# Optimization experiments

Hardware: AMD Instinct MI355X
Metric: run time of the kernel (lower is better)

The kernel has to match this reference:

```python
import jax, jax.numpy as jnp
import numpy as np

B, S, D = 2, 2048, 1024
H, DQK, DV = 16, 64, 64

def setup_inputs() -> dict:
    key = jax.random.key(0)
    k1, k2, k3, k4, k5 = jax.random.split(key, 5)
    scale_in = 1.0 / np.sqrt(D)
    scale_v = 1.0 / np.sqrt(H * DV)
    return {
        "x":   jax.random.normal(k1, (B, S, D), dtype=jnp.float32),
        "W_q": jax.random.uniform(k2, (D, H * DQK), minval=-scale_in, maxval=scale_in, dtype=jnp.float32),
        "W_k": jax.random.uniform(k3, (D, H * DQK), minval=-scale_in, maxval=scale_in, dtype=jnp.float32),
        "W_v": jax.random.uniform(k4, (D, H * DV), minval=-scale_in, maxval=scale_in, dtype=jnp.float32),
        "W_o": jax.random.uniform(k5, (H * DV, D), minval=-scale_v, maxval=scale_v, dtype=jnp.float32),
    }

def reference(x, W_q, W_k, W_v, W_o):
    b, s, _ = x.shape
    # projections -> [B, H, S, d]
    Q = (x @ W_q).reshape(b, s, H, DQK).transpose(0, 2, 1, 3)
    K = (x @ W_k).reshape(b, s, H, DQK).transpose(0, 2, 1, 3)
    V = (x @ W_v).reshape(b, s, H, DV).transpose(0, 2, 1, 3)
    scores = jnp.einsum('bhqd,bhkd->bhqk', Q, K) / np.sqrt(DQK).astype(np.float32)
    causal_mask = jnp.triu(jnp.ones((s, s), dtype=bool), k=1)  # True above diagonal
    scores = jnp.where(causal_mask[None, None], -jnp.inf, scores)
    attn = jax.nn.softmax(scores, axis=-1)
    out = jnp.einsum('bhqk,bhkd->bhqd', attn, V)  # [B,H,S,DV]
    out = out.transpose(0, 2, 1, 3).reshape(b, s, H * DV)
    return out @ W_o
```

## Files before the change

kernel.cpp:

```cpp
#include <hip/hip_runtime.h>


typedef float  f32x4  __attribute__((ext_vector_type(4)));
typedef __bf16 bf16x8 __attribute__((ext_vector_type(8)));

__device__ __forceinline__ unsigned short f2bf(float f) {
    __bf16 h = (__bf16)f;
    return __builtin_bit_cast(unsigned short, h);
}

__device__ __forceinline__ void gld16(unsigned short* lds, const unsigned short* g) {
    __builtin_amdgcn_global_load_lds(
        (const __attribute__((address_space(1))) void*)g,
        (__attribute__((address_space(3))) void*)lds, 16, 0, 0);
}

__global__ __launch_bounds__(256) void castx(const float* __restrict__ x,
                                             unsigned short* __restrict__ xb) {
    size_t i = ((size_t)blockIdx.x * 256 + threadIdx.x) * 4;
    float4 v = *(const float4*)(x + i);
    ushort4 o;
    o.x = f2bf(v.x); o.y = f2bf(v.y); o.z = f2bf(v.z); o.w = f2bf(v.w);
    *(ushort4*)(xb + i) = o;
}

__global__ __launch_bounds__(256) void wtrans(const float* __restrict__ W0,
                                              const float* __restrict__ W1,
                                              const float* __restrict__ W2,
                                              const float* __restrict__ W3,
                                              unsigned short* __restrict__ WT) {
    __shared__ float T[64][65];
    const int z = blockIdx.z;
    const float* W = (z == 0) ? W0 : (z == 1) ? W1 : (z == 2) ? W2 : W3;
    const int k0 = blockIdx.y * 64, n0 = blockIdx.x * 64;
    const int tid = threadIdx.x;
#pragma unroll
    for (int i = 0; i < 4; i++) {
        int c = tid + i * 256;
        int r = c >> 4, col = (c & 15) * 4;
        float4 v = *(const float4*)(W + (size_t)(k0 + r) * 1024 + n0 + col);
        T[r][col] = v.x; T[r][col + 1] = v.y; T[r][col + 2] = v.z; T[r][col + 3] = v.w;
    }
    __syncthreads();
    unsigned short* out = WT + (size_t)z * 1024 * 1024;
#pragma unroll
    for (int i = 0; i < 2; i++) {
        int c = tid + i * 256;
        int nr = c >> 3, koff = (c & 7) * 8;
        union { unsigned short us[8]; uint4 v; } pk;
#pragma unroll
        for (int j = 0; j < 8; j++) pk.us[j] = f2bf(T[koff + j][nr]);
        *(uint4*)(out + (size_t)(n0 + nr) * 1024 + k0 + koff) = pk.v;
    }
}

__global__ __launch_bounds__(256) void gemm_qkv(const unsigned short* __restrict__ A,
                                                const unsigned short* __restrict__ WTall,
                                                unsigned short* __restrict__ outq,
                                                unsigned short* __restrict__ Vp) {
    __shared__ unsigned short As[128 * 32];
    __shared__ unsigned short Bs[128 * 32];
    const int tid = threadIdx.x;
    const int w = tid >> 6, lane = tid & 63, quad = lane >> 4, ln = lane & 15;

    const int blk = blockIdx.x;
    const int n0 = ((blk >> 3) & 7) * 128;
    const int g  = ((blk >> 6) << 3) | (blk & 7);
    const int z  = g >> 5;
    const int m0 = (g & 31) * 128;

    const unsigned short* BT = WTall + (size_t)z * (1024 * 1024);
    const float scl = (z == 0) ? 0.180336878f : 1.0f;
    const bool swp = (z < 2);

    const int lr = lane >> 2;
    const int lc = ((lane & 3) ^ (lr & 3)) * 8;
    const int fsw = (quad ^ (ln & 3)) * 8;

    const f32x4 z4 = {0.f, 0.f, 0.f, 0.f};
    f32x4 acc[4][4];
#pragma unroll
    for (int i = 0; i < 4; i++)
#pragma unroll
        for (int j = 0; j < 4; j++) acc[i][j] = z4;

    const int wm = (w & 1) * 64, wn = (w >> 1) * 64;
    const int R0 = w * 32, R1 = w * 32 + 16;

    for (int k0 = 0; k0 < 1024; k0 += 32) {
        __syncthreads();
        gld16(As + R0 * 32, A  + (size_t)(m0 + R0 + lr) * 1024 + k0 + lc);
        gld16(As + R1 * 32, A  + (size_t)(m0 + R1 + lr) * 1024 + k0 + lc);
        gld16(Bs + R0 * 32, BT + (size_t)(n0 + R0 + lr) * 1024 + k0 + lc);
        gld16(Bs + R1 * 32, BT + (size_t)(n0 + R1 + lr) * 1024 + k0 + lc);
        __syncthreads();
        bf16x8 af[4], bfr[4];
#pragma unroll
        for (int t = 0; t < 4; t++)
            af[t] = *(const bf16x8*)&As[(wm + t * 16 + ln) * 32 + fsw];
#pragma unroll
        for (int t = 0; t < 4; t++)
            bfr[t] = *(const bf16x8*)&Bs[(wn + t * 16 + ln) * 32 + fsw];
        if (swp) {
#pragma unroll
            for (int tm = 0; tm < 4; tm++)
#pragma unroll
                for (int tn = 0; tn < 4; tn++)
                    acc[tm][tn] = __builtin_amdgcn_mfma_f32_16x16x32_bf16(
                        bfr[tn], af[tm], acc[tm][tn], 0, 0, 0);
        } else {
#pragma unroll
            for (int tm = 0; tm < 4; tm++)
#pragma unroll
                for (int tn = 0; tn < 4; tn++)
                    acc[tm][tn] = __builtin_amdgcn_mfma_f32_16x16x32_bf16(
                        af[tm], bfr[tn], acc[tm][tn], 0, 0, 0);
        }
    }

    if (swp) {
#pragma unroll
        for (int tm = 0; tm < 4; tm++)
#pragma unroll
            for (int tn = 0; tn < 4; tn++) {
                int mg = m0 + wm + tm * 16 + ln;
                int nb = n0 + wn + tn * 16 + quad * 4;
                int b = mg >> 11, s = mg & 2047, h = nb >> 6, dd = nb & 63;
                ushort4 o;
                o.x = f2bf(acc[tm][tn][0] * scl);
                o.y = f2bf(acc[tm][tn][1] * scl);
                o.z = f2bf(acc[tm][tn][2] * scl);
                o.w = f2bf(acc[tm][tn][3] * scl);
                size_t zoff = (size_t)z * (4096 * 1024);
                *(ushort4*)(outq + zoff + (((size_t)(b * 16 + h) * 2048 + s) << 6) + dd) = o;
            }
    } else {
#pragma unroll
        for (int tm = 0; tm < 4; tm++)
#pragma unroll
            for (int tn = 0; tn < 4; tn++) {
                int mg = m0 + wm + tm * 16 + quad * 4;
                int ng = n0 + wn + tn * 16 + ln;
                int b = mg >> 11, h = ng >> 6, dd = ng & 63;
                int sblk = (mg & 2047) & ~63;
                int cb = tm >> 1, t16 = tm & 1;
                int pp = cb * 32 + quad * 8 + t16 * 4;
                ushort4 o;
                o.x = f2bf(acc[tm][tn][0]);
                o.y = f2bf(acc[tm][tn][1]);
                o.z = f2bf(acc[tm][tn][2]);
                o.w = f2bf(acc[tm][tn][3]);
                *(ushort4*)(Vp + ((size_t)(b * 16 + h) * 64 + dd) * 2048 + sblk + pp) = o;
            }
    }
}

__global__ __launch_bounds__(256) void gemm_o(const unsigned short* __restrict__ A,
                                              const unsigned short* __restrict__ BT,
                                              float* __restrict__ outf) {
    __shared__ unsigned short As[128 * 32];
    __shared__ unsigned short Bs[128 * 32];
    const int tid = threadIdx.x;
    const int w = tid >> 6, lane = tid & 63, quad = lane >> 4, ln = lane & 15;

    const int blk = blockIdx.x;
    const int n0 = ((blk >> 3) & 7) * 128;
    const int m0 = (((blk >> 6) << 3) | (blk & 7)) * 128;

    const int lr = lane >> 2;
    const int lc = ((lane & 3) ^ (lr & 3)) * 8;
    const int fsw = (quad ^ (ln & 3)) * 8;

    const f32x4 z4 = {0.f, 0.f, 0.f, 0.f};
    f32x4 acc[4][4];
#pragma unroll
    for (int i = 0; i < 4; i++)
#pragma unroll
        for (int j = 0; j < 4; j++) acc[i][j] = z4;

    const int wm = (w & 1) * 64, wn = (w >> 1) * 64;
    const int R0 = w * 32, R1 = w * 32 + 16;

    for (int k0 = 0; k0 < 1024; k0 += 32) {
        __syncthreads();
        gld16(As + R0 * 32, A  + (size_t)(m0 + R0 + lr) * 1024 + k0 + lc);
        gld16(As + R1 * 32, A  + (size_t)(m0 + R1 + lr) * 1024 + k0 + lc);
        gld16(Bs + R0 * 32, BT + (size_t)(n0 + R0 + lr) * 1024 + k0 + lc);
        gld16(Bs + R1 * 32, BT + (size_t)(n0 + R1 + lr) * 1024 + k0 + lc);
        __syncthreads();
        bf16x8 af[4], bfr[4];
#pragma unroll
        for (int t = 0; t < 4; t++)
            af[t] = *(const bf16x8*)&As[(wm + t * 16 + ln) * 32 + fsw];
#pragma unroll
        for (int t = 0; t < 4; t++)
            bfr[t] = *(const bf16x8*)&Bs[(wn + t * 16 + ln) * 32 + fsw];
#pragma unroll
        for (int tm = 0; tm < 4; tm++)
#pragma unroll
            for (int tn = 0; tn < 4; tn++)
                acc[tm][tn] = __builtin_amdgcn_mfma_f32_16x16x32_bf16(
                    bfr[tn], af[tm], acc[tm][tn], 0, 0, 0);
    }

#pragma unroll
    for (int tm = 0; tm < 4; tm++)
#pragma unroll
        for (int tn = 0; tn < 4; tn++) {
            int mg = m0 + wm + tm * 16 + ln;
            int nb = n0 + wn + tn * 16 + quad * 4;
            *(f32x4*)(outf + (size_t)mg * 1024 + nb) = acc[tm][tn];
        }
}

__global__ __launch_bounds__(256, 4) void flash(const unsigned short* __restrict__ Qb,
                                                const unsigned short* __restrict__ Kb,
                                                const unsigned short* __restrict__ Vpb,
                                                unsigned short* __restrict__ AO) {
    __shared__ __align__(16) unsigned short Ks[64 * 64];
    __shared__ __align__(16) unsigned short Vs[64 * 64];
    const int tid = threadIdx.x, w = tid >> 6, lane = tid & 63;
    const int qd = lane >> 4, ln = lane & 15;
    const int lr = lane >> 3;
    const int lchunk = (lane & 7) ^ lr;
    const int psw = (qd ^ (ln & 7)) * 8;

    const int blk = blockIdx.x;
    const int j = blk >> 3;
    const int bh = (blk & 7) + ((j >> 5) << 3);
    const int idx = j & 31;
    const int pr = idx >> 1;
    const int qi = (idx & 1) ? (16 + pr) : (15 - pr);
    const int qt0 = qi * 64;

    const unsigned short* Kg = Kb  + (size_t)bh * 2048 * 64;
    const unsigned short* Vg = Vpb + (size_t)bh * 64 * 2048;

    bf16x8 aq[2];
    {
        const unsigned short* Qrow = Qb + ((size_t)bh * 2048 + qt0 + w * 16 + ln) * 64 + qd * 8;
        aq[0] = *(const bf16x8*)(Qrow);
        aq[1] = *(const bf16x8*)(Qrow + 32);
    }

    const f32x4 z4 = {0.f, 0.f, 0.f, 0.f};
    f32x4 Oc[4];
#pragma unroll
    for (int td = 0; td < 4; td++) Oc[td] = z4;
    float lsum = 0.f;

    const int qrow = qt0 + w * 16 + ln;
    const int qmin = qt0 + w * 16;
    const int qmax = qmin + 15;
    const int kend = qt0 + 64;

    for (int k0 = 0; k0 < kend; k0 += 64) {
        __syncthreads();
        {
            const unsigned short* kg = Kg + (size_t)(k0 + w * 16 + lr) * 64 + lchunk * 8;
            gld16(Ks + (w * 16) * 64, kg);
            gld16(Ks + (w * 16 + 8) * 64, kg + 8 * 64);
            const unsigned short* vg = Vg + (size_t)(w * 16 + lr) * 2048 + k0 + lchunk * 8;
            gld16(Vs + (w * 16) * 64, vg);
            gld16(Vs + (w * 16 + 8) * 64, vg + 8 * 2048);
        }
        __syncthreads();

        f32x4 sc[4];
#pragma unroll
        for (int t = 0; t < 4; t++) {
            sc[t] = z4;
            if (k0 + t * 16 <= qmax) {
                int off = (t * 16 + ln) * 64 + psw;
                bf16x8 bk0 = *(const bf16x8*)&Ks[off];
                bf16x8 bk1 = *(const bf16x8*)&Ks[off ^ 32];
                sc[t] = __builtin_amdgcn_mfma_f32_16x16x32_bf16(bk0, aq[0], sc[t], 0, 0, 0);
                sc[t] = __builtin_amdgcn_mfma_f32_16x16x32_bf16(bk1, aq[1], sc[t], 0, 0, 0);
            }
        }

        unsigned int pk[4][2];
#pragma unroll
        for (int t = 0; t < 4; t++) {
            if (k0 + t * 16 > qmax) { pk[t][0] = 0u; pk[t][1] = 0u; continue; }
            float e[4];
#pragma unroll
            for (int r = 0; r < 4; r++) e[r] = __builtin_amdgcn_exp2f(sc[t][r]);
            if (k0 + t * 16 + 15 > qmin) {
#pragma unroll
                for (int r = 0; r < 4; r++)
                    if (k0 + t * 16 + qd * 4 + r > qrow) e[r] = 0.f;
            }
            lsum += (e[0] + e[1]) + (e[2] + e[3]);
            pk[t][0] = (unsigned int)f2bf(e[0]) | ((unsigned int)f2bf(e[1]) << 16);
            pk[t][1] = (unsigned int)f2bf(e[2]) | ((unsigned int)f2bf(e[3]) << 16);
        }

        union { unsigned int u[4]; bf16x8 v; } apu0, apu1;
        apu0.u[0] = pk[0][0]; apu0.u[1] = pk[0][1]; apu0.u[2] = pk[1][0]; apu0.u[3] = pk[1][1];
        apu1.u[0] = pk[2][0]; apu1.u[1] = pk[2][1]; apu1.u[2] = pk[3][0]; apu1.u[3] = pk[3][1];
#pragma unroll
        for (int td = 0; td < 4; td++) {
            int voff = (td * 16 + ln) * 64 + psw;
            bf16x8 av0 = *(const bf16x8*)&Vs[voff];
            bf16x8 av1 = *(const bf16x8*)&Vs[voff ^ 32];
            Oc[td] = __builtin_amdgcn_mfma_f32_16x16x32_bf16(av0, apu0.v, Oc[td], 0, 0, 0);
            Oc[td] = __builtin_amdgcn_mfma_f32_16x16x32_bf16(av1, apu1.v, Oc[td], 0, 0, 0);
        }
    }

    lsum += __shfl_xor(lsum, 16);
    lsum += __shfl_xor(lsum, 32);
    const float inv = 1.0f / lsum;

    const int bz = bh >> 4, h = bh & 15;
    const int rowg = qt0 + w * 16 + ln;
    unsigned short* aorow = AO + ((size_t)(bz * 2048 + rowg) << 10) + h * 64 + qd * 4;
#pragma unroll
    for (int td = 0; td < 4; td++) {
        ushort4 o;
        o.x = f2bf(Oc[td][0] * inv);
        o.y = f2bf(Oc[td][1] * inv);
        o.z = f2bf(Oc[td][2] * inv);
        o.w = f2bf(Oc[td][3] * inv);
        *(ushort4*)(aorow + td * 16) = o;
    }
}

extern "C" void kernel_launch(void* const* d_in, const int* in_sizes, int n_in,
                              void* d_out, int out_size, void* d_ws, size_t ws_size,
                              hipStream_t stream) {
    const float* x  = (const float*)d_in[0];
    const float* Wq = (const float*)d_in[1];
    const float* Wk = (const float*)d_in[2];
    const float* Wv = (const float*)d_in[3];
    const float* Wo = (const float*)d_in[4];
    float* out = (float*)d_out;

    unsigned short* xb  = (unsigned short*)d_ws;
    unsigned short* WT  = xb  + (size_t)4096 * 1024;
    unsigned short* Qb  = WT  + (size_t)4 * 1024 * 1024;
    unsigned short* Kb  = Qb  + (size_t)4096 * 1024;
    unsigned short* Vb  = Kb  + (size_t)4096 * 1024;
    unsigned short* Vpb = Vb  + (size_t)4096 * 1024;
    unsigned short* AO  = Vpb + (size_t)4096 * 1024;

    castx<<<4096, 256, 0, stream>>>(x, xb);
    wtrans<<<dim3(16, 16, 4), 256, 0, stream>>>(Wq, Wk, Wv, Wo, WT);
    gemm_qkv<<<dim3(768), 256, 0, stream>>>(xb, WT, Qb, Vpb);
    flash<<<dim3(1024), 256, 0, stream>>>(Qb, Kb, Vpb, AO);
    gemm_o<<<dim3(256), 256, 0, stream>>>(AO, WT + (size_t)3 * 1024 * 1024, out);
}
```

Before: 206.1 us.

## Double-buffer K/V tiles in flash attention and pair causal blocks

The K/V shared-memory tiles become two buffers. The next 64-key tile is issued with async global-to-LDS loads while the current tile is computed, which leaves one barrier per iteration instead of two. The block-to-(head, query tile) mapping also changes so that adjacent blocks pair a long causal row tile with a short one, to balance work across the grid. This doubles LDS use per block and relies on the barrier waiting for outstanding LDS-DMA loads before the buffer is read.

```diff
diff --git a/kernel.cpp b/kernel.cpp
--- a/kernel.cpp
+++ b/kernel.cpp
@@ -217,8 +217,8 @@
                                                 const unsigned short* __restrict__ Kb,
                                                 const unsigned short* __restrict__ Vpb,
                                                 unsigned short* __restrict__ AO) {
-    __shared__ __align__(16) unsigned short Ks[64 * 64];
-    __shared__ __align__(16) unsigned short Vs[64 * 64];
+    __shared__ __align__(16) unsigned short Ks[2][64 * 64];
+    __shared__ __align__(16) unsigned short Vs[2][64 * 64];
     const int tid = threadIdx.x, w = tid >> 6, lane = tid & 63;
     const int qd = lane >> 4, ln = lane & 15;
     const int lr = lane >> 3;
@@ -226,11 +226,10 @@
     const int psw = (qd ^ (ln & 7)) * 8;
 
     const int blk = blockIdx.x;
-    const int j = blk >> 3;
-    const int bh = (blk & 7) + ((j >> 5) << 3);
-    const int idx = j & 31;
-    const int pr = idx >> 1;
-    const int qi = (idx & 1) ? (16 + pr) : (15 - pr);
+    const int pairid = blk >> 1;
+    const int bh = pairid & 31;
+    const int jj = pairid >> 5;
+    const int qi = (blk & 1) ? jj : (31 - jj);
     const int qt0 = qi * 64;
 
     const unsigned short* Kg = Kb  + (size_t)bh * 2048 * 64;
@@ -254,17 +253,22 @@
     const int qmax = qmin + 15;
     const int kend = qt0 + 64;
 
+#define FLASH_STAGE(buf, kk)                                                          \
+    {                                                                                 \
+        const unsigned short* kg = Kg + (size_t)((kk) + w * 16 + lr) * 64 + lchunk * 8; \
+        gld16(&Ks[buf][(w * 16) * 64], kg);                                           \
+        gld16(&Ks[buf][(w * 16 + 8) * 64], kg + 8 * 64);                              \
+        const unsigned short* vg = Vg + (size_t)(w * 16 + lr) * 2048 + (kk) + lchunk * 8; \
+        gld16(&Vs[buf][(w * 16) * 64], vg);                                           \
+        gld16(&Vs[buf][(w * 16 + 8) * 64], vg + 8 * 2048);                            \
+    }
+
+    FLASH_STAGE(0, 0);
+    int cur = 0;
+
     for (int k0 = 0; k0 < kend; k0 += 64) {
         __syncthreads();
-        {
-            const unsigned short* kg = Kg + (size_t)(k0 + w * 16 + lr) * 64 + lchunk * 8;
-            gld16(Ks + (w * 16) * 64, kg);
-            gld16(Ks + (w * 16 + 8) * 64, kg + 8 * 64);
-            const unsigned short* vg = Vg + (size_t)(w * 16 + lr) * 2048 + k0 + lchunk * 8;
-            gld16(Vs + (w * 16) * 64, vg);
-            gld16(Vs + (w * 16 + 8) * 64, vg + 8 * 2048);
-        }
-        __syncthreads();
+        if (k0 + 64 < kend) FLASH_STAGE(cur ^ 1, k0 + 64);
 
         f32x4 sc[4];
 #pragma unroll
@@ -272,8 +276,8 @@
             sc[t] = z4;
             if (k0 + t * 16 <= qmax) {
                 int off = (t * 16 + ln) * 64 + psw;
-                bf16x8 bk0 = *(const bf16x8*)&Ks[off];
-                bf16x8 bk1 = *(const bf16x8*)&Ks[off ^ 32];
+                bf16x8 bk0 = *(const bf16x8*)&Ks[cur][off];
+                bf16x8 bk1 = *(const bf16x8*)&Ks[cur][off ^ 32];
                 sc[t] = __builtin_amdgcn_mfma_f32_16x16x32_bf16(bk0, aq[0], sc[t], 0, 0, 0);
                 sc[t] = __builtin_amdgcn_mfma_f32_16x16x32_bf16(bk1, aq[1], sc[t], 0, 0, 0);
             }
@@ -302,12 +306,14 @@
 #pragma unroll
         for (int td = 0; td < 4; td++) {
             int voff = (td * 16 + ln) * 64 + psw;
-            bf16x8 av0 = *(const bf16x8*)&Vs[voff];
-            bf16x8 av1 = *(const bf16x8*)&Vs[voff ^ 32];
+            bf16x8 av0 = *(const bf16x8*)&Vs[cur][voff];
+            bf16x8 av1 = *(const bf16x8*)&Vs[cur][voff ^ 32];
             Oc[td] = __builtin_amdgcn_mfma_f32_16x16x32_bf16(av0, apu0.v, Oc[td], 0, 0, 0);
             Oc[td] = __builtin_amdgcn_mfma_f32_16x16x32_bf16(av1, apu1.v, Oc[td], 0, 0, 0);
         }
-    }
+        cur ^= 1;
+    }
+#undef FLASH_STAGE
 
     lsum += __shfl_xor(lsum, 16);
     lsum += __shfl_xor(lsum, 32);
```

New measurement: 197.4 us. 1.04x faster.
